# Kernel tuning notes

Hardware: AMD Instinct MI355X
Metric: run time of the kernel (lower is better)

Reference implementation:

```python
import jax, jax.numpy as jnp
import numpy as np

HIDDEN = 4096
N_HEADS = 16
HEAD_DIM = HIDDEN // N_HEADS  # 256
ROTARY_DIM = 64
ROPE_THETA = 10000.0


def _rope_cos_sin(positions):
    # positions: [S] int -> cos/sin: [S, ROTARY_DIM//2]
    inv_freq = 1.0 / (ROPE_THETA ** (jnp.arange(0, ROTARY_DIM, 2, dtype=jnp.float32) / ROTARY_DIM))
    angles = positions.astype(jnp.float32)[:, None] * inv_freq[None, :]
    return jnp.cos(angles), jnp.sin(angles)


def _apply_rope_interleaved(x, cos, sin):
    # x: [B, S, H, D]; rotate first ROTARY_DIM dims, GPT-J (non-neox) interleaved pairs
    xr = x[..., :ROTARY_DIM]
    x1 = xr[..., 0::2]
    x2 = xr[..., 1::2]
    c = cos[None, :, None, :]
    s = sin[None, :, None, :]
    o1 = x1 * c - x2 * s
    o2 = x1 * s + x2 * c
    rot = jnp.stack([o1, o2], axis=-1).reshape(xr.shape)
    return jnp.concatenate([rot, x[..., ROTARY_DIM:]], axis=-1)


def setup_inputs() -> dict:
    key = jax.random.key(0)
    k1, k2, k3 = jax.random.split(key, 3)
    B, S = 2, 2048
    hidden_states = jax.random.normal(k1, (B, S, HIDDEN), dtype=jnp.float32)
    positions = jnp.arange(S, dtype=jnp.int32)
    w_qkv = jax.random.normal(k2, (3 * HIDDEN, HIDDEN), dtype=jnp.float32) * 0.02
    w_out = jax.random.normal(k3, (HIDDEN, HIDDEN), dtype=jnp.float32) * 0.02
    return {"hidden_states": hidden_states, "positions": positions, "w_qkv": w_qkv, "w_out": w_out}


def reference(hidden_states, positions, w_qkv, w_out):
    B, S, H = hidden_states.shape
    qkv = jnp.einsum("bsh,oh->bso", hidden_states, w_qkv)  # [B,S,3H]
    q, k, v = jnp.split(qkv, 3, axis=-1)
    q = q.reshape(B, S, N_HEADS, HEAD_DIM)
    k = k.reshape(B, S, N_HEADS, HEAD_DIM)
    v = v.reshape(B, S, N_HEADS, HEAD_DIM)
    cos, sin = _rope_cos_sin(positions)
    q = _apply_rope_interleaved(q, cos, sin)
    k = _apply_rope_interleaved(k, cos, sin)
    scale = HEAD_DIM ** -0.5
    scores = jnp.einsum("bqhd,bkhd->bhqk", q, k) * scale  # [B,nh,S,S]
    causal = jnp.tril(jnp.ones((S, S), dtype=bool))
    scores = jnp.where(causal[None, None], scores, jnp.finfo(scores.dtype).min)
    probs = jax.nn.softmax(scores, axis=-1)
    attn = jnp.einsum("bhqk,bkhd->bqhd", probs, v).reshape(B, S, H)
    return jnp.einsum("bsh,oh->bso", attn, w_out)
```

## Files before the change

### kernel.cpp

```cpp
#include <hip/hip_runtime.h>

typedef __attribute__((ext_vector_type(8))) short short8;
typedef __attribute__((ext_vector_type(4))) float f32x4;

__device__ __forceinline__ unsigned short f2bf(float f) {
    union { float f; unsigned int u; } v; v.f = f;
    unsigned int u = v.u;
    unsigned int r = (u + 0x7FFFu + ((u >> 16) & 1u)) >> 16;
    return (unsigned short)r;
}
__device__ __forceinline__ float bf2f(unsigned short u) {
    union { unsigned int u; float f; } v; v.u = ((unsigned int)u) << 16;
    return v.f;
}
__device__ __forceinline__ void load_lds16(const void* g, void* l) {
    __builtin_amdgcn_global_load_lds(
        (const __attribute__((address_space(1))) void*)g,
        (__attribute__((address_space(3))) void*)l, 16, 0, 0);
}
#define BAR() asm volatile("s_barrier" ::: "memory")
#define WAITV(n) asm volatile("s_waitcnt vmcnt(" #n ")" ::: "memory")

__device__ __forceinline__ int swz(int o) { return o ^ ((o >> 3) & 0x70); }

__global__ __launch_bounds__(256) void conv_bf16(const float* __restrict__ in,
                                                 unsigned short* __restrict__ out, int n4) {
    int i = blockIdx.x * 256 + threadIdx.x;
    if (i >= n4) return;
    float4 v = ((const float4*)in)[i];
    ushort4 o;
    o.x = f2bf(v.x); o.y = f2bf(v.y); o.z = f2bf(v.z); o.w = f2bf(v.w);
    ((ushort4*)out)[i] = o;
}

template <bool OUT_BF16>
__global__ __launch_bounds__(512, 2) void gemm256(const unsigned short* __restrict__ A,
                                                  const unsigned short* __restrict__ B,
                                                  void* __restrict__ Cv,
                                                  int M, int N, int K, int NBN) {
    __shared__ __align__(16) char smem[131072];
    const int tid = threadIdx.x;
    const int lane = tid & 63, wv = tid >> 6;
    const int wm = wv >> 2, wn = wv & 3;
    const int fr = lane & 15, fo = (lane >> 4) * 8;

    const int nwg = gridDim.x, bid = blockIdx.x;
    const int q = nwg >> 3, r = nwg & 7, xcd = bid & 7, lid = bid >> 3;
    const int wg = (xcd < r ? xcd * (q + 1) : r * (q + 1) + (xcd - r) * q) + lid;
    const int bm = wg / NBN, bn = wg % NBN;

    const unsigned short* gA = A + (size_t)bm * 256 * K;
    const unsigned short* gB = B + (size_t)bn * 256 * K;

    int srow[2][2], scol[2][2];
#pragma unroll
    for (int h = 0; h < 2; ++h)
#pragma unroll
        for (int rr = 0; rr < 2; ++rr) {
            int o = h * 16384 + rr * 8192 + tid * 16;
            int osw = swz(o);
            srow[h][rr] = osw >> 7;
            scol[h][rr] = (osw & 127) >> 1;
        }

    f32x4 acc[8][4] = {};
    short8 a[4][2], b[4][2];

    auto STAGE = [&](const unsigned short* g, int regionBase, int h, int t) {
#pragma unroll
        for (int rr = 0; rr < 2; ++rr)
            load_lds16(g + (size_t)srow[h][rr] * K + t * 64 + scol[h][rr],
                       smem + regionBase + h * 16384 + rr * 8192 + tid * 16);
    };
    auto RDA = [&](int bufBase, int mh) {
#pragma unroll
        for (int mf = 0; mf < 4; ++mf)
#pragma unroll
            for (int ks = 0; ks < 2; ++ks) {
                int o = swz((wm * 128 + mh * 64 + mf * 16 + fr) * 128 + (ks * 32 + fo) * 2);
                a[mf][ks] = *(const short8*)(smem + bufBase + o);
            }
    };
    auto RDB = [&](int bufBase, int nh) {
#pragma unroll
        for (int jj = 0; jj < 2; ++jj)
#pragma unroll
            for (int ks = 0; ks < 2; ++ks) {
                int o = swz((wn * 64 + (nh * 2 + jj) * 16 + fr) * 128 + (ks * 32 + fo) * 2);
                b[nh * 2 + jj][ks] = *(const short8*)(smem + bufBase + 32768 + o);
            }
    };
    auto MM = [&](int mh, int nh) {
        __builtin_amdgcn_s_setprio(1);
#pragma unroll
        for (int mf = 0; mf < 4; ++mf)
#pragma unroll
            for (int jj = 0; jj < 2; ++jj)
#pragma unroll
                for (int ks = 0; ks < 2; ++ks)
                    acc[mh * 4 + mf][nh * 2 + jj] = __builtin_amdgcn_mfma_f32_16x16x32_bf16(
                        a[mf][ks], b[nh * 2 + jj][ks], acc[mh * 4 + mf][nh * 2 + jj], 0, 0, 0);
        __builtin_amdgcn_s_setprio(0);
    };

    const int A0 = 0, B0 = 32768, A1 = 65536, B1 = 98304;

    STAGE(gA, A0, 0, 0); STAGE(gA, A0, 1, 0);
    STAGE(gB, B0, 0, 0); STAGE(gB, B0, 1, 0);
    STAGE(gB, B1, 0, 1); STAGE(gB, B1, 1, 1);
    STAGE(gA, A1, 0, 1); STAGE(gA, A1, 1, 1);
    WAITV(8);
    BAR();
    RDA(A0, 0);
    RDB(A0, 0);

    const int NIT = K >> 7;
    for (int i = 0; i < NIT; ++i) {
        const bool last = (i == NIT - 1);
        const int t2 = 2 * i + 2, t3 = 2 * i + 3;
        RDB(A0, 1);
        MM(0, 0);
        if (i > 0) STAGE(gA, A1, 1, 2 * i + 1);
        BAR();
        MM(0, 1);
        RDA(A0, 1);
        BAR();
        MM(1, 1);
        if (!last) {
            STAGE(gB, B0, 0, t2);
            WAITV(2);
        } else {
            WAITV(0);
        }
        BAR();
        MM(1, 0);
        RDA(A1, 0); RDB(A1, 0);
        if (!last) { STAGE(gB, B0, 1, t2); STAGE(gA, A0, 0, t2); }
        BAR();
        RDB(A1, 1);
        MM(0, 0);
        if (!last) STAGE(gA, A0, 1, t2);
        BAR();
        MM(0, 1);
        RDA(A1, 1);
        BAR();
        MM(1, 1);
        if (!last) {
            STAGE(gB, B1, 0, t3);
            WAITV(2);
        }
        BAR();
        MM(1, 0);
        if (!last) {
            RDA(A0, 0); RDB(A0, 0);
            STAGE(gB, B1, 1, t3); STAGE(gA, A1, 0, t3);
        }
        BAR();
    }

    const size_t row0 = (size_t)bm * 256 + wm * 128 + ((lane >> 4) << 2);
    const int col0 = bn * 256 + wn * 64 + fr;
#pragma unroll
    for (int mf = 0; mf < 8; ++mf)
#pragma unroll
        for (int nf = 0; nf < 4; ++nf)
#pragma unroll
            for (int j = 0; j < 4; ++j) {
                size_t idx = (row0 + mf * 16 + j) * (size_t)N + col0 + nf * 16;
                if (OUT_BF16) ((unsigned short*)Cv)[idx] = f2bf(acc[mf][nf][j]);
                else          ((float*)Cv)[idx] = acc[mf][nf][j];
            }
}

__global__ __launch_bounds__(256) void rope_repack(const unsigned short* __restrict__ qkv,
                                                   const int* __restrict__ positions,
                                                   unsigned short* __restrict__ qp,
                                                   unsigned short* __restrict__ kp) {
    int r = blockIdx.x * 4 + (threadIdx.x >> 6);
    int h = r & 15, s = (r >> 4) & 2047, b = r >> 15;
    int d = (threadIdx.x & 63) * 4;
    const unsigned short* src = qkv + (size_t)(b * 2048 + s) * 12288 + h * 256 + d;
    ushort4 q = *(const ushort4*)src;
    ushort4 k = *(const ushort4*)(src + 4096);
    if (d < 64) {
        float pos = (float)positions[s];
        const float LF = 0.4152410118609203f;
        float i0 = (float)(d >> 1);
        float a0 = pos * exp2f(-i0 * LF);
        float a1 = pos * exp2f(-(i0 + 1.0f) * LF);
        float c0 = cosf(a0), s0 = sinf(a0), c1 = cosf(a1), s1 = sinf(a1);
        float qx = bf2f(q.x), qy = bf2f(q.y), qz = bf2f(q.z), qw = bf2f(q.w);
        q.x = f2bf(qx * c0 - qy * s0); q.y = f2bf(qx * s0 + qy * c0);
        q.z = f2bf(qz * c1 - qw * s1); q.w = f2bf(qz * s1 + qw * c1);
        float kx = bf2f(k.x), ky = bf2f(k.y), kz = bf2f(k.z), kw = bf2f(k.w);
        k.x = f2bf(kx * c0 - ky * s0); k.y = f2bf(kx * s0 + ky * c0);
        k.z = f2bf(kz * c1 - kw * s1); k.w = f2bf(kz * s1 + kw * c1);
    }
    size_t dst = ((size_t)((b * 16 + h) * 2048 + s)) * 256 + d;
    *(ushort4*)&qp[dst] = q;
    *(ushort4*)&kp[dst] = k;
}

__global__ __launch_bounds__(256) void v_transpose(const unsigned short* __restrict__ qkv,
                                                   unsigned short* __restrict__ vt) {
    int bid = blockIdx.x;
    int dt = bid & 3, st = (bid >> 2) & 31, bh = bid >> 7;
    int b = bh >> 4, h = bh & 15;
    __shared__ unsigned short t[64][72];
    int tid = threadIdx.x;
#pragma unroll
    for (int rep = 0; rep < 16; ++rep) {
        int idx = rep * 256 + tid;
        int r = idx >> 6, c = idx & 63;
        t[r][c] = qkv[(size_t)(b * 2048 + st * 64 + r) * 12288 + 8192 + h * 256 + dt * 64 + c];
    }
    __syncthreads();
#pragma unroll
    for (int rep = 0; rep < 16; ++rep) {
        int idx = rep * 256 + tid;
        int r = idx >> 6, c = idx & 63;
        vt[(size_t)(bh * 256 + dt * 64 + r) * 2048 + st * 64 + c] = t[c][r];
    }
}

__global__ __launch_bounds__(256) void attn_fwd(const unsigned short* __restrict__ Qp,
                                                const unsigned short* __restrict__ Kp,
                                                const unsigned short* __restrict__ Vt,
                                                unsigned short* __restrict__ Oa) {
    __shared__ __align__(16) unsigned short Ks[32 * 256];
    __shared__ __align__(16) unsigned short Vs[256 * 32];
    __shared__ __align__(16) unsigned short Ps[4][16 * 32];
    const int tid = threadIdx.x, lane = tid & 63, wv = tid >> 6;
    const int bh = blockIdx.x, qt = blockIdx.y;
    const int fr = lane & 15, fo = (lane >> 4) * 8;
    const unsigned short* Qb = Qp + (size_t)bh * 2048 * 256;
    const unsigned short* Kb = Kp + (size_t)bh * 2048 * 256;
    const unsigned short* Vb = Vt + (size_t)bh * 256 * 2048;
    const int qbase = qt * 64 + wv * 16;

    short8 qf[8];
#pragma unroll
    for (int c = 0; c < 8; ++c)
        qf[c] = *(const short8*)&Qb[(size_t)(qbase + fr) * 256 + c * 32 + fo];

    f32x4 o_acc[16] = {};
    float m_run[4] = {-1e30f, -1e30f, -1e30f, -1e30f};
    float l_run[4] = {0.f, 0.f, 0.f, 0.f};

    const int nkv = qt * 64 + 64;
    for (int kv0 = 0; kv0 < nkv; kv0 += 32) {
#pragma unroll
        for (int i = 0; i < 4; ++i) {
            int eb = (wv * 4 + i) * 512;
            load_lds16(&Kb[(size_t)(kv0 + (eb >> 8) + (lane >> 5)) * 256 + (lane & 31) * 8], &Ks[eb]);
        }
#pragma unroll
        for (int i = 0; i < 4; ++i) {
            int eb = (wv * 4 + i) * 512;
            load_lds16(&Vb[(size_t)((eb >> 5) + (lane >> 2)) * 2048 + kv0 + (lane & 3) * 8], &Vs[eb]);
        }
        __syncthreads();

        f32x4 sc[2] = {};
#pragma unroll
        for (int t = 0; t < 2; ++t)
#pragma unroll
            for (int c = 0; c < 8; ++c) {
                short8 kf = *(const short8*)&Ks[(t * 16 + fr) * 256 + c * 32 + fo];
                sc[t] = __builtin_amdgcn_mfma_f32_16x16x32_bf16(qf[c], kf, sc[t], 0, 0, 0);
            }

        float sv[2][4];
#pragma unroll
        for (int j = 0; j < 4; ++j) {
            int qi = qbase + ((lane >> 4) << 2) + j;
#pragma unroll
            for (int t = 0; t < 2; ++t) {
                float x = sc[t][j] * 0.0625f;
                int kvi = kv0 + t * 16 + fr;
                sv[t][j] = (kvi > qi) ? -1e30f : x;
            }
            float pm = fmaxf(sv[0][j], sv[1][j]);
#pragma unroll
            for (int off = 1; off < 16; off <<= 1)
                pm = fmaxf(pm, __shfl_xor(pm, off));
            float mn = fmaxf(m_run[j], pm);
            float al = __expf(m_run[j] - mn);
            m_run[j] = mn;
            float rs = 0.f;
#pragma unroll
            for (int t = 0; t < 2; ++t) {
                float p = __expf(sv[t][j] - mn);
                rs += p;
                Ps[wv][(((lane >> 4) << 2) + j) * 32 + t * 16 + fr] = f2bf(p);
            }
#pragma unroll
            for (int off = 1; off < 16; off <<= 1)
                rs += __shfl_xor(rs, off);
            l_run[j] = l_run[j] * al + rs;
#pragma unroll
            for (int n = 0; n < 16; ++n) o_acc[n][j] *= al;
        }

        short8 pf = *(const short8*)&Ps[wv][fr * 32 + fo];
#pragma unroll
        for (int n = 0; n < 16; ++n) {
            short8 vf = *(const short8*)&Vs[(n * 16 + fr) * 32 + fo];
            o_acc[n] = __builtin_amdgcn_mfma_f32_16x16x32_bf16(pf, vf, o_acc[n], 0, 0, 0);
        }
        __syncthreads();
    }

    const int b = bh >> 4, h = bh & 15;
#pragma unroll
    for (int j = 0; j < 4; ++j) {
        float inv = 1.0f / l_run[j];
        int qrow = qbase + ((lane >> 4) << 2) + j;
        size_t base = ((size_t)(b * 2048 + qrow)) * 4096 + h * 256;
#pragma unroll
        for (int n = 0; n < 16; ++n)
            Oa[base + n * 16 + fr] = f2bf(o_acc[n][j] * inv);
    }
}

extern "C" void kernel_launch(void* const* d_in, const int* in_sizes, int n_in,
                              void* d_out, int out_size, void* d_ws, size_t ws_size,
                              hipStream_t stream) {
    const float* hidden = (const float*)d_in[0];
    const int* positions = (const int*)d_in[1];
    const float* w_qkv = (const float*)d_in[2];
    const float* w_out = (const float*)d_in[3];
    float* out = (float*)d_out;

    const size_t MB32 = 33554432;
    char* ws = (char*)d_ws;
    unsigned short* hidden_bf = (unsigned short*)ws;
    unsigned short* wqkv_bf   = (unsigned short*)(ws + MB32);
    unsigned short* qkv_bf    = (unsigned short*)(ws + 4 * MB32);
    unsigned short* qp  = wqkv_bf;
    unsigned short* kp  = wqkv_bf + 16777216;
    unsigned short* vtp = wqkv_bf + 33554432;
    unsigned short* attn_bf = hidden_bf;
    unsigned short* wout_bf = qkv_bf;

    conv_bf16<<<16384, 256, 0, stream>>>(hidden, hidden_bf, 4194304);
    conv_bf16<<<49152, 256, 0, stream>>>(w_qkv, wqkv_bf, 12582912);

    gemm256<true><<<16 * 48, 512, 0, stream>>>(hidden_bf, wqkv_bf, qkv_bf, 4096, 12288, 4096, 48);

    rope_repack<<<16384, 256, 0, stream>>>(qkv_bf, positions, qp, kp);
    v_transpose<<<4096, 256, 0, stream>>>(qkv_bf, vtp);

    attn_fwd<<<dim3(32, 32), 256, 0, stream>>>(qp, kp, vtp, attn_bf);

    conv_bf16<<<16384, 256, 0, stream>>>(w_out, wout_bf, 4194304);
    gemm256<false><<<16 * 16, 512, 0, stream>>>(attn_bf, wout_bf, out, 4096, 4096, 4096, 16);
}
```

Measured before the change: 867.2 us.

## Switch GEMM to 32x32x16 MFMA, restage pipeline, and defer softmax rescaling

The projection GEMM now uses 32x32x16 bf16 MFMA tiles instead of 16x16x32. Larger tiles mean fewer LDS fragment reads per FLOP, and the LDS-staging/barrier schedule and epilogue store mapping are rewritten to match. Separately, the attention kernel's online softmax skips the max update and the accumulator rescale unless some row's tile max exceeds the running max by more than 8, which removes most rescale multiplies. That threshold trick relies on exponentials staying bounded by e^8 in bf16/fp32, and the reworked GEMM schedule adds more barriers per iteration.

```diff
diff --git a/kernel.cpp b/kernel.cpp
--- a/kernel.cpp
+++ b/kernel.cpp
@@ -2,6 +2,7 @@
 
 typedef __attribute__((ext_vector_type(8))) short short8;
 typedef __attribute__((ext_vector_type(4))) float f32x4;
+typedef __attribute__((ext_vector_type(16))) float f32x16;
 
 __device__ __forceinline__ unsigned short f2bf(float f) {
     union { float f; unsigned int u; } v; v.f = f;
@@ -42,7 +43,7 @@
     const int tid = threadIdx.x;
     const int lane = tid & 63, wv = tid >> 6;
     const int wm = wv >> 2, wn = wv & 3;
-    const int fr = lane & 15, fo = (lane >> 4) * 8;
+    const int lr = lane & 31, hi = lane >> 5;
 
     const int nwg = gridDim.x, bid = blockIdx.x;
     const int q = nwg >> 3, r = nwg & 7, xcd = bid & 7, lid = bid >> 3;
@@ -63,8 +64,9 @@
             scol[h][rr] = (osw & 127) >> 1;
         }
 
-    f32x4 acc[8][4] = {};
-    short8 a[4][2], b[4][2];
+    f32x16 acc[4][2] = {};
+    short8 a[2][2][2];
+    short8 b[2][4];
 
     auto STAGE = [&](const unsigned short* g, int regionBase, int h, int t) {
 #pragma unroll
@@ -72,103 +74,89 @@
             load_lds16(g + (size_t)srow[h][rr] * K + t * 64 + scol[h][rr],
                        smem + regionBase + h * 16384 + rr * 8192 + tid * 16);
     };
-    auto RDA = [&](int bufBase, int mh) {
-#pragma unroll
-        for (int mf = 0; mf < 4; ++mf)
-#pragma unroll
-            for (int ks = 0; ks < 2; ++ks) {
-                int o = swz((wm * 128 + mh * 64 + mf * 16 + fr) * 128 + (ks * 32 + fo) * 2);
-                a[mf][ks] = *(const short8*)(smem + bufBase + o);
-            }
-    };
-    auto RDB = [&](int bufBase, int nh) {
-#pragma unroll
-        for (int jj = 0; jj < 2; ++jj)
-#pragma unroll
-            for (int ks = 0; ks < 2; ++ks) {
-                int o = swz((wn * 64 + (nh * 2 + jj) * 16 + fr) * 128 + (ks * 32 + fo) * 2);
-                b[nh * 2 + jj][ks] = *(const short8*)(smem + bufBase + 32768 + o);
-            }
-    };
-    auto MM = [&](int mh, int nh) {
-        __builtin_amdgcn_s_setprio(1);
-#pragma unroll
-        for (int mf = 0; mf < 4; ++mf)
-#pragma unroll
-            for (int jj = 0; jj < 2; ++jj)
-#pragma unroll
-                for (int ks = 0; ks < 2; ++ks)
-                    acc[mh * 4 + mf][nh * 2 + jj] = __builtin_amdgcn_mfma_f32_16x16x32_bf16(
-                        a[mf][ks], b[nh * 2 + jj][ks], acc[mh * 4 + mf][nh * 2 + jj], 0, 0, 0);
-        __builtin_amdgcn_s_setprio(0);
-    };
+
+#define AB_OFF(row, ks16) swz((((row)) << 7) + (ks16) * 32 + hi * 16)
+#define RD_A(s, mh, kp, base) do { \
+    a[s][0][0] = *(const short8*)(smem + (base) + AB_OFF(wm * 128 + (mh) * 64 + lr,      (kp) * 2));     \
+    a[s][0][1] = *(const short8*)(smem + (base) + AB_OFF(wm * 128 + (mh) * 64 + lr,      (kp) * 2 + 1)); \
+    a[s][1][0] = *(const short8*)(smem + (base) + AB_OFF(wm * 128 + (mh) * 64 + 32 + lr, (kp) * 2));     \
+    a[s][1][1] = *(const short8*)(smem + (base) + AB_OFF(wm * 128 + (mh) * 64 + 32 + lr, (kp) * 2 + 1)); } while (0)
+#define RD_B(kp, base) do { \
+    b[0][(kp) * 2]     = *(const short8*)(smem + (base) + 32768 + AB_OFF(wn * 64 + lr,      (kp) * 2));     \
+    b[0][(kp) * 2 + 1] = *(const short8*)(smem + (base) + 32768 + AB_OFF(wn * 64 + lr,      (kp) * 2 + 1)); \
+    b[1][(kp) * 2]     = *(const short8*)(smem + (base) + 32768 + AB_OFF(wn * 64 + 32 + lr, (kp) * 2));     \
+    b[1][(kp) * 2 + 1] = *(const short8*)(smem + (base) + 32768 + AB_OFF(wn * 64 + 32 + lr, (kp) * 2 + 1)); } while (0)
+#define MM8(s, mh, kp) do { \
+    __builtin_amdgcn_s_setprio(1); \
+    acc[(mh)*2][0]   = __builtin_amdgcn_mfma_f32_32x32x16_bf16(a[s][0][0], b[0][(kp)*2],   acc[(mh)*2][0],   0, 0, 0); \
+    acc[(mh)*2][1]   = __builtin_amdgcn_mfma_f32_32x32x16_bf16(a[s][0][0], b[1][(kp)*2],   acc[(mh)*2][1],   0, 0, 0); \
+    acc[(mh)*2+1][0] = __builtin_amdgcn_mfma_f32_32x32x16_bf16(a[s][1][0], b[0][(kp)*2],   acc[(mh)*2+1][0], 0, 0, 0); \
+    acc[(mh)*2+1][1] = __builtin_amdgcn_mfma_f32_32x32x16_bf16(a[s][1][0], b[1][(kp)*2],   acc[(mh)*2+1][1], 0, 0, 0); \
+    acc[(mh)*2][0]   = __builtin_amdgcn_mfma_f32_32x32x16_bf16(a[s][0][1], b[0][(kp)*2+1], acc[(mh)*2][0],   0, 0, 0); \
+    acc[(mh)*2][1]   = __builtin_amdgcn_mfma_f32_32x32x16_bf16(a[s][0][1], b[1][(kp)*2+1], acc[(mh)*2][1],   0, 0, 0); \
+    acc[(mh)*2+1][0] = __builtin_amdgcn_mfma_f32_32x32x16_bf16(a[s][1][1], b[0][(kp)*2+1], acc[(mh)*2+1][0], 0, 0, 0); \
+    acc[(mh)*2+1][1] = __builtin_amdgcn_mfma_f32_32x32x16_bf16(a[s][1][1], b[1][(kp)*2+1], acc[(mh)*2+1][1], 0, 0, 0); \
+    __builtin_amdgcn_s_setprio(0); } while (0)
 
     const int A0 = 0, B0 = 32768, A1 = 65536, B1 = 98304;
 
     STAGE(gA, A0, 0, 0); STAGE(gA, A0, 1, 0);
     STAGE(gB, B0, 0, 0); STAGE(gB, B0, 1, 0);
     STAGE(gB, B1, 0, 1); STAGE(gB, B1, 1, 1);
-    STAGE(gA, A1, 0, 1); STAGE(gA, A1, 1, 1);
-    WAITV(8);
+    WAITV(4);
     BAR();
-    RDA(A0, 0);
-    RDB(A0, 0);
 
     const int NIT = K >> 7;
     for (int i = 0; i < NIT; ++i) {
         const bool last = (i == NIT - 1);
-        const int t2 = 2 * i + 2, t3 = 2 * i + 3;
-        RDB(A0, 1);
-        MM(0, 0);
-        if (i > 0) STAGE(gA, A1, 1, 2 * i + 1);
+        const int t1 = 2 * i + 1, t2 = 2 * i + 2, t3 = 2 * i + 3;
+        RD_A(0, 0, 0, A0); RD_B(0, A0);
+        STAGE(gA, A1, 0, t1);
+        BAR(); MM8(0, 0, 0); BAR();
+        RD_A(1, 0, 1, A0); RD_B(1, A0);
+        STAGE(gA, A1, 1, t1);
+        BAR(); MM8(1, 0, 1); BAR();
+        RD_A(0, 1, 1, A0);
+        if (!last) STAGE(gB, B0, 0, t2);
+        BAR(); MM8(0, 1, 1); BAR();
+        RD_A(1, 1, 0, A0);
+        if (!last) STAGE(gB, B0, 1, t2);
+        BAR(); MM8(1, 1, 0);
+        if (last) WAITV(0); else WAITV(4);
         BAR();
-        MM(0, 1);
-        RDA(A0, 1);
+        RD_A(0, 0, 0, A1); RD_B(0, A1);
+        if (!last) STAGE(gA, A0, 0, t2);
+        BAR(); MM8(0, 0, 0); BAR();
+        RD_A(1, 0, 1, A1); RD_B(1, A1);
+        if (!last) STAGE(gA, A0, 1, t2);
+        BAR(); MM8(1, 0, 1); BAR();
+        RD_A(0, 1, 1, A1);
+        if (!last) STAGE(gB, B1, 0, t3);
+        BAR(); MM8(0, 1, 1); BAR();
+        RD_A(1, 1, 0, A1);
+        if (!last) STAGE(gB, B1, 1, t3);
+        BAR(); MM8(1, 1, 0);
+        if (!last) WAITV(4);
         BAR();
-        MM(1, 1);
-        if (!last) {
-            STAGE(gB, B0, 0, t2);
-            WAITV(2);
-        } else {
-            WAITV(0);
-        }
-        BAR();
-        MM(1, 0);
-        RDA(A1, 0); RDB(A1, 0);
-        if (!last) { STAGE(gB, B0, 1, t2); STAGE(gA, A0, 0, t2); }
-        BAR();
-        RDB(A1, 1);
-        MM(0, 0);
-        if (!last) STAGE(gA, A0, 1, t2);
-        BAR();
-        MM(0, 1);
-        RDA(A1, 1);
-        BAR();
-        MM(1, 1);
-        if (!last) {
-            STAGE(gB, B1, 0, t3);
-            WAITV(2);
-        }
-        BAR();
-        MM(1, 0);
-        if (!last) {
-            RDA(A0, 0); RDB(A0, 0);
-            STAGE(gB, B1, 1, t3); STAGE(gA, A1, 0, t3);
-        }
-        BAR();
-    }
-
-    const size_t row0 = (size_t)bm * 256 + wm * 128 + ((lane >> 4) << 2);
-    const int col0 = bn * 256 + wn * 64 + fr;
-#pragma unroll
-    for (int mf = 0; mf < 8; ++mf)
-#pragma unroll
-        for (int nf = 0; nf < 4; ++nf)
-#pragma unroll
-            for (int j = 0; j < 4; ++j) {
-                size_t idx = (row0 + mf * 16 + j) * (size_t)N + col0 + nf * 16;
-                if (OUT_BF16) ((unsigned short*)Cv)[idx] = f2bf(acc[mf][nf][j]);
-                else          ((float*)Cv)[idx] = acc[mf][nf][j];
+    }
+#undef AB_OFF
+#undef RD_A
+#undef RD_B
+#undef MM8
+
+    const size_t row0 = (size_t)bm * 256 + wm * 128 + hi * 4;
+    const int col0 = bn * 256 + wn * 64 + lr;
+#pragma unroll
+    for (int mt = 0; mt < 4; ++mt)
+#pragma unroll
+        for (int nt = 0; nt < 2; ++nt)
+#pragma unroll
+            for (int r2 = 0; r2 < 16; ++r2) {
+                size_t row = row0 + mt * 32 + (r2 & 3) + ((r2 >> 2) << 3);
+                size_t idx = row * (size_t)N + col0 + nt * 32;
+                float v = acc[mt][nt][r2];
+                if (OUT_BF16) ((unsigned short*)Cv)[idx] = f2bf(v);
+                else          ((float*)Cv)[idx] = v;
             }
 }
 
@@ -270,7 +258,7 @@
                 sc[t] = __builtin_amdgcn_mfma_f32_16x16x32_bf16(qf[c], kf, sc[t], 0, 0, 0);
             }
 
-        float sv[2][4];
+        float sv[2][4], pm[4];
 #pragma unroll
         for (int j = 0; j < 4; ++j) {
             int qi = qbase + ((lane >> 4) << 2) + j;
@@ -280,26 +268,38 @@
                 int kvi = kv0 + t * 16 + fr;
                 sv[t][j] = (kvi > qi) ? -1e30f : x;
             }
-            float pm = fmaxf(sv[0][j], sv[1][j]);
+            float p = fmaxf(sv[0][j], sv[1][j]);
 #pragma unroll
             for (int off = 1; off < 16; off <<= 1)
-                pm = fmaxf(pm, __shfl_xor(pm, off));
-            float mn = fmaxf(m_run[j], pm);
-            float al = __expf(m_run[j] - mn);
-            m_run[j] = mn;
+                p = fmaxf(p, __shfl_xor(p, off));
+            pm[j] = p;
+        }
+        bool need = (pm[0] > m_run[0] + 8.f) | (pm[1] > m_run[1] + 8.f) |
+                    (pm[2] > m_run[2] + 8.f) | (pm[3] > m_run[3] + 8.f);
+        if (__any(need)) {
+#pragma unroll
+            for (int j = 0; j < 4; ++j) {
+                float mn = fmaxf(m_run[j], pm[j]);
+                float al = __expf(m_run[j] - mn);
+                m_run[j] = mn;
+                l_run[j] *= al;
+#pragma unroll
+                for (int n = 0; n < 16; ++n) o_acc[n][j] *= al;
+            }
+        }
+#pragma unroll
+        for (int j = 0; j < 4; ++j) {
             float rs = 0.f;
 #pragma unroll
             for (int t = 0; t < 2; ++t) {
-                float p = __expf(sv[t][j] - mn);
+                float p = __expf(sv[t][j] - m_run[j]);
                 rs += p;
                 Ps[wv][(((lane >> 4) << 2) + j) * 32 + t * 16 + fr] = f2bf(p);
             }
 #pragma unroll
             for (int off = 1; off < 16; off <<= 1)
                 rs += __shfl_xor(rs, off);
-            l_run[j] = l_run[j] * al + rs;
-#pragma unroll
-            for (int n = 0; n < 16; ++n) o_acc[n][j] *= al;
+            l_run[j] += rs;
         }
 
         short8 pf = *(const short8*)&Ps[wv][fr * 32 + fo];
```

New measurement: 884.4 us. About the same (+2.0%).
